# Performance work log

Measured on AMD Instinct MI355X. Metric: run time of the kernel, lower is better.

Reference implementation:

```python
import jax, jax.numpy as jnp
import numpy as np

B, N, L, H, K = 65536, 32, 8, 256, 8
RMIN, RMAX = -10.0, 10.0
MIN_BIN, MIN_SLOPE = 1e-4, 1e-4
P = 3 * K + 1  # params per feature per spline


def setup_inputs() -> dict:
    key = jax.random.key(0)
    ks = jax.random.split(key, 20)
    def rn(k, shape, s=0.05):
        return (jax.random.normal(k, shape, dtype=jnp.float32) * s)
    inp = {
        'x': jax.random.normal(ks[0], (B, N), dtype=jnp.float32),
        'sc_scale': 1.0 + rn(ks[1], (L, N)),
        'sc_shift': rn(ks[2], (L, N)),
        'W_in': rn(ks[3], (L, N, H)), 'b_in': rn(ks[4], (L, H)),
        'W1a': rn(ks[5], (L, H, H)), 'b1a': rn(ks[6], (L, H)),
        'W1b': rn(ks[7], (L, H, H)), 'b1b': rn(ks[8], (L, H)),
        'W2a': rn(ks[9], (L, H, H)), 'b2a': rn(ks[10], (L, H)),
        'W2b': rn(ks[11], (L, H, H)), 'b2b': rn(ks[12], (L, H)),
        'W_out': rn(ks[13], (L, H, N * P)), 'b_out': rn(ks[14], (L, N * P)),
        'perms': jnp.asarray(np.stack([np.random.RandomState(i).permutation(N) for i in range(L)]).astype(np.int32)),
    }
    return inp


def _conditioner(mx, Wi, bi, W1a, b1a, W1b, b1b, W2a, b2a, W2b, b2b, Wo, bo):
    # mx: [B, N] masked input -> [B, N, P] spline params
    h = mx @ Wi + bi
    r = jax.nn.relu(jax.nn.relu(h @ W1a + b1a) @ W1b + b1b)
    h = h + r
    r = jax.nn.relu(jax.nn.relu(h @ W2a + b2a) @ W2b + b2b)
    h = h + r
    h = jax.nn.relu(h)
    out = h @ Wo + bo
    return out.reshape(mx.shape[0], N, P)


def _rqs_forward(x, params):
    # x: [B, N]; params: [B, N, 3K+1]. distrax RationalQuadraticSpline forward.
    uw, uh, ud = params[..., :K], params[..., K:2 * K], params[..., 2 * K:]
    total = RMAX - RMIN
    w = jax.nn.softmax(uw, axis=-1) * (total - K * MIN_BIN) + MIN_BIN
    hgt = jax.nn.softmax(uh, axis=-1) * (total - K * MIN_BIN) + MIN_BIN
    zpad = jnp.zeros_like(w[..., :1])
    xp = RMIN + jnp.concatenate([zpad, jnp.cumsum(w, -1)], -1)   # [B,N,K+1]
    yp = RMIN + jnp.concatenate([zpad, jnp.cumsum(hgt, -1)], -1)
    offset = float(np.log(np.expm1(1.0 - MIN_SLOPE)))
    d = jax.nn.softplus(ud + offset) + MIN_SLOPE                  # [B,N,K+1]
    inside = (x > RMIN) & (x < RMAX)
    xc = jnp.clip(x, RMIN, RMAX)
    # per-element bin search (knot positions vary per element)
    idx = jnp.clip(jnp.sum((xc[..., None] >= xp).astype(jnp.int32), -1) - 1, 0, K - 1)
    g = lambda a, i: jnp.take_along_axis(a, i[..., None], -1)[..., 0]
    xk, xk1 = g(xp, idx), g(xp, idx + 1)
    yk, yk1 = g(yp, idx), g(yp, idx + 1)
    dk, dk1 = g(d, idx), g(d, idx + 1)
    bw = xk1 - xk
    bh = yk1 - yk
    s = bh / bw
    z = jnp.clip((xc - xk) / bw, 0.0, 1.0)
    zz = z * (1.0 - z)
    denom = s + (dk1 + dk - 2.0 * s) * zz
    y = yk + bh * (s * z * z + dk * zz) / denom
    ld = 2.0 * jnp.log(s) + jnp.log(dk1 * z * z + 2.0 * s * zz + dk * (1.0 - z) ** 2) - 2.0 * jnp.log(denom)
    return jnp.where(inside, y, x), jnp.where(inside, ld, 0.0)


def reference(x, sc_scale, sc_shift, W_in, b_in, W1a, b1a, W1b, b1b,
              W2a, b2a, W2b, b2b, W_out, b_out, perms):
    mask0 = (jnp.arange(N) % 2).astype(bool)  # True = identity (masked)
    logdet = jnp.zeros(x.shape[0], dtype=x.dtype)
    for i in range(L):
        # Permute
        x = x[:, perms[i]]
        # Scalar affine on all features (mask_all = all-False coupling)
        x = x * sc_scale[i] + sc_shift[i]
        logdet = logdet + jnp.sum(jnp.log(jnp.abs(sc_scale[i])))
        # RQ-spline masked coupling
        mask = mask0 if i % 2 == 0 else ~mask0
        mx = jnp.where(mask, x, 0.0)
        params = _conditioner(mx, W_in[i], b_in[i], W1a[i], b1a[i], W1b[i], b1b[i],
                              W2a[i], b2a[i], W2b[i], b2b[i], W_out[i], b_out[i])
        y, ld = _rqs_forward(x, params)
        x = jnp.where(mask, x, y)
        logdet = logdet + jnp.sum(jnp.where(mask, 0.0, ld), axis=-1)
    # standard-normal base log prob
    logp = -0.5 * jnp.sum(x * x, axis=-1) - 0.5 * N * float(np.log(2.0 * np.pi))
    return logp + logdet
```

## Files before the change

### kernel.cpp

```cpp
#include <hip/hip_runtime.h>
#include <hip/hip_bf16.h>

typedef __attribute__((ext_vector_type(8))) short bf16x8;
typedef __attribute__((ext_vector_type(16))) float f32x16;
typedef __attribute__((ext_vector_type(2))) float f32x2;

#define DEVFN __device__ __forceinline__

constexpr int NFEAT = 32, NLAYER = 8, HID = 256;
constexpr int HS  = 264;
constexpr int MXS = 40;
constexpr int XS  = 33;
constexpr int PS  = 132;
constexpr int WIN_E  = 2 * 256 * 16;
constexpr int WH_E   = 16 * 256 * 16;
constexpr int WOUT_E = 16 * 512 * 16;
constexpr int LAYER_E = WIN_E + 4 * WH_E + WOUT_E;
constexpr size_t WT_BYTES = (size_t)LAYER_E * NLAYER * 2;
constexpr size_t WS_NEEDED = WT_BYTES + NLAYER * 512 * 4 + 4;

constexpr float MIN_BIN = 1e-4f, MIN_SLOPE = 1e-4f;
constexpr float SOFTPLUS_OFF = 0.5411666f;
constexpr float WSCALE = 20.0f - 8.0f * MIN_BIN;

DEVFN unsigned short bf16r(float f) {
    unsigned u = __float_as_uint(f);
    u += 0x7fffu + ((u >> 16) & 1u);
    return (unsigned short)(u >> 16);
}
#if defined(__gfx950__) && __has_builtin(__builtin_amdgcn_cvt_pk_bf16_f32)
DEVFN unsigned pack2(float a, float b) {
    auto r = __builtin_amdgcn_cvt_pk_bf16_f32(a, b);
    return __builtin_bit_cast(unsigned, r);
}
#else
DEVFN unsigned pack2(float a, float b) {
    return (unsigned)bf16r(a) | ((unsigned)bf16r(b) << 16);
}
#endif
DEVFN float bflo(unsigned v) { return __uint_as_float(v << 16); }
DEVFN float bfhi(unsigned v) { return __uint_as_float(v & 0xffff0000u); }
DEVFN float frcp(float x) { return __builtin_amdgcn_rcpf(x); }
DEVFN f32x2 vmax0(f32x2 v) {
#if __has_builtin(__builtin_elementwise_max)
    return __builtin_elementwise_max(v, (f32x2){0.f, 0.f});
#else
    return (f32x2){fmaxf(v.x, 0.f), fmaxf(v.y, 0.f)};
#endif
}

__global__ __launch_bounds__(256) void prep_kernel(
    const float* __restrict__ Win, const float* __restrict__ W1a, const float* __restrict__ W1b,
    const float* __restrict__ W2a, const float* __restrict__ W2b, const float* __restrict__ Wout,
    const float* __restrict__ bout, const float* __restrict__ scS,
    short* __restrict__ wt, float* __restrict__ bo_t, float* __restrict__ sld)
{
    __shared__ float lb[16 * 800];
    const int b = blockIdx.x, t = threadIdx.x;
    if (b < 16) {
        int l = b >> 1, ks = b & 1;
        const float* src = Win + l * 32 * 256 + ks * 16 * 256;
#pragma unroll
        for (int i = 0; i < 16; i++) { int idx = t + i * 256; lb[idx] = src[idx]; }
        __syncthreads();
        short* dst = wt + (size_t)l * LAYER_E + ks * 4096;
#pragma unroll
        for (int i = 0; i < 16; i++) {
            int o = t + i * 256; int n = o >> 4, kk = o & 15;
            dst[o] = (short)bf16r(lb[kk * 256 + n]);
        }
    } else if (b < 528) {
        int id = b - 16; int l = id >> 6, mat = (id >> 4) & 3, ks = id & 15;
        const float* mats[4] = {W1a, W1b, W2a, W2b};
        const float* src = mats[mat] + l * 65536 + ks * 16 * 256;
#pragma unroll
        for (int i = 0; i < 16; i++) { int idx = t + i * 256; lb[idx] = src[idx]; }
        __syncthreads();
        short* dst = wt + (size_t)l * LAYER_E + WIN_E + mat * WH_E + ks * 4096;
#pragma unroll
        for (int i = 0; i < 16; i++) {
            int o = t + i * 256; int n = o >> 4, kk = o & 15;
            dst[o] = (short)bf16r(lb[kk * 256 + n]);
        }
    } else if (b < 656) {
        int id = b - 528; int l = id >> 4, ks = id & 15; int par = l & 1;
        const float* src = Wout + (size_t)l * 256 * 800 + ks * 16 * 800;
        for (int k = 0; k < 16; k++)
            for (int c = t; c < 800; c += 256) lb[k * 800 + c] = src[k * 800 + c];
        __syncthreads();
        short* dst = wt + (size_t)l * LAYER_E + WIN_E + 4 * WH_E + ks * 8192;
#pragma unroll
        for (int i = 0; i < 32; i++) {
            int o = t + i * 256; int c = o >> 4, kk = o & 15;
            int u = c >> 5, p = c & 31;
            float v = (p < 25) ? lb[kk * 800 + (2 * u + par) * 25 + p] : 0.0f;
            dst[o] = (short)bf16r(v);
        }
    } else {
#pragma unroll
        for (int i = 0; i < 16; i++) {
            int idx = t + i * 256;
            int l = idx >> 9, c = idx & 511, u = c >> 5, p = c & 31;
            bo_t[idx] = (p < 25) ? bout[l * 800 + (2 * u + (l & 1)) * 25 + p] : 0.0f;
        }
        lb[t] = logf(fabsf(scS[t]));
        __syncthreads();
        for (int s = 128; s > 0; s >>= 1) { if (t < s) lb[t] += lb[t + s]; __syncthreads(); }
        if (t == 0) *sld = lb[0];
    }
}

template<int KSTEPS, int NSUB>
DEVFN void gemm_flip(const short* __restrict__ wt, int ntot, int nbase,
                     const unsigned short* __restrict__ B, int bs,
                     f32x16 (&acc)[NSUB][2])
{
    constexpr int D = (KSTEPS < 4) ? KSTEPS : 4;
    const int lane = threadIdx.x & 63;
    const int l31 = lane & 31, l5 = lane >> 5;
    const bf16x8* __restrict__ w8 = (const bf16x8*)wt;
    const int wb = (nbase + l31) * 2 + l5;
    const int krow = ntot * 2;
    bf16x8 a[D][NSUB];
#pragma unroll
    for (int p = 0; p < D; p++)
#pragma unroll
        for (int s = 0; s < NSUB; s++) a[p][s] = w8[(size_t)p * krow + wb + s * 64];
    const unsigned short* bp = B + l31 * bs + l5 * 8;
#pragma unroll
    for (int k = 0; k < KSTEPS; k++) {
        bf16x8 b0 = *(const bf16x8*)(bp + k * 16);
        bf16x8 b1 = *(const bf16x8*)(bp + 32 * bs + k * 16);
#pragma unroll
        for (int s = 0; s < NSUB; s++) {
            acc[s][0] = __builtin_amdgcn_mfma_f32_32x32x16_bf16(a[k % D][s], b0, acc[s][0], 0, 0, 0);
            acc[s][1] = __builtin_amdgcn_mfma_f32_32x32x16_bf16(a[k % D][s], b1, acc[s][1], 0, 0, 0);
        }
        if (k + D < KSTEPS) {
#pragma unroll
            for (int s = 0; s < NSUB; s++) a[k % D][s] = w8[(size_t)(k + D) * krow + wb + s * 64];
        }
    }
}

DEVFN void binit(f32x16& a, const float* __restrict__ bias)
{
    const int q = (threadIdx.x >> 5) & 1;
    const float* bp = bias + 4 * q;
#pragma unroll
    for (int g = 0; g < 4; g++) {
        float4 b = *(const float4*)(bp + 8 * g);
        a[4*g+0] = b.x; a[4*g+1] = b.y; a[4*g+2] = b.z; a[4*g+3] = b.w;
    }
}

template<int MODE>
DEVFN void store_h(const f32x16& v, unsigned short* buf, int m0, int n0)
{
    const int lane = threadIdx.x & 63;
    const int m = m0 + (lane & 31);
    const int q = lane >> 5;
    unsigned short* rowp = buf + m * HS + n0 + 4 * q;
#pragma unroll
    for (int g = 0; g < 4; g++) {
        f32x2 r0 = {v[4*g+0], v[4*g+1]};
        f32x2 r1 = {v[4*g+2], v[4*g+3]};
        if (MODE >= 1) { r0 = vmax0(r0); r1 = vmax0(r1); }
        unsigned short* dst = rowp + 8 * g;
        if (MODE >= 2) {
            uint2 old = *(const uint2*)dst;
            r0 += (f32x2){bflo(old.x), bfhi(old.x)};
            r1 += (f32x2){bflo(old.y), bfhi(old.y)};
            if (MODE == 3) { r0 = vmax0(r0); r1 = vmax0(r1); }
        }
        uint2 pk;
        pk.x = pack2(r0.x, r0.y);
        pk.y = pack2(r1.x, r1.y);
        *(uint2*)dst = pk;
    }
}

DEVFN void store_p(const f32x16& v, float* pbuf, int m0, int c0)
{
    const int lane = threadIdx.x & 63;
    const int m = m0 + (lane & 31);
    const int q = lane >> 5;
    float* rowp = pbuf + m * PS + c0 + 4 * q;
#pragma unroll
    for (int g = 0; g < 4; g++)
        *(float4*)(rowp + 8 * g) = make_float4(v[4*g], v[4*g+1], v[4*g+2], v[4*g+3]);
}

__global__ __launch_bounds__(256, 2) void flow_kernel(
    const float* __restrict__ x_in, const float* __restrict__ scS, const float* __restrict__ scB,
    const float* __restrict__ bin, const float* __restrict__ b1a, const float* __restrict__ b1b,
    const float* __restrict__ b2a, const float* __restrict__ b2b,
    const int* __restrict__ perms,
    const short* __restrict__ wt, const float* __restrict__ bo_t, const float* __restrict__ sld,
    float* __restrict__ out)
{
    __shared__ __align__(16) unsigned short hS[64 * HS];
    __shared__ __align__(16) float uS[8448];
    __shared__ float xS[64 * XS];
    __shared__ float redS[256];

    const int tid = threadIdx.x;
    const int wave = tid >> 6;
    const size_t rowbase = (size_t)blockIdx.x * 64;
    unsigned short* tS  = (unsigned short*)uS;
    unsigned short* mxS = (unsigned short*)uS;
    float* pS = uS;

#pragma unroll
    for (int i = 0; i < 8; i++) {
        int g = tid + i * 256;
        xS[(g >> 5) * XS + (g & 31)] = x_in[rowbase * NFEAT + g];
    }
    float ld_acc = 0.0f;
    __syncthreads();

    const int nbase = wave * 64;

#pragma unroll 1
    for (int l = 0; l < NLAYER; l++) {
        const int par = l & 1;
        const short* wb = wt + (size_t)l * LAYER_E;

        {
            int j = tid & 31; int r0 = (tid >> 5) * 8;
            int pj = perms[l * 32 + j];
            float sc = scS[l * 32 + j], sh = scB[l * 32 + j];
            float vals[8];
#pragma unroll
            for (int r = 0; r < 8; r++) vals[r] = xS[(r0 + r) * XS + pj] * sc + sh;
            __syncthreads();
            int keep = ((j & 1) != par);
#pragma unroll
            for (int r = 0; r < 8; r++) {
                xS[(r0 + r) * XS + j] = vals[r];
                mxS[(r0 + r) * MXS + j] = keep ? bf16r(vals[r]) : (unsigned short)0;
            }
            __syncthreads();
        }
        {
            f32x16 acc[2][2];
            binit(acc[0][0], bin + l * 256 + nbase);      binit(acc[0][1], bin + l * 256 + nbase);
            binit(acc[1][0], bin + l * 256 + nbase + 32); binit(acc[1][1], bin + l * 256 + nbase + 32);
            gemm_flip<2, 2>(wb, 256, nbase, mxS, MXS, acc);
#pragma unroll
            for (int s = 0; s < 2; s++) {
                store_h<0>(acc[s][0], hS, 0,  nbase + s * 32);
                store_h<0>(acc[s][1], hS, 32, nbase + s * 32);
            }
            __syncthreads();
        }
        {
            f32x16 acc[2][2];
            binit(acc[0][0], b1a + l * 256 + nbase);      binit(acc[0][1], b1a + l * 256 + nbase);
            binit(acc[1][0], b1a + l * 256 + nbase + 32); binit(acc[1][1], b1a + l * 256 + nbase + 32);
            gemm_flip<16, 2>(wb + WIN_E, 256, nbase, hS, HS, acc);
#pragma unroll
            for (int s = 0; s < 2; s++) {
                store_h<1>(acc[s][0], tS, 0,  nbase + s * 32);
                store_h<1>(acc[s][1], tS, 32, nbase + s * 32);
            }
            __syncthreads();
        }
        {
            f32x16 acc[2][2];
            binit(acc[0][0], b1b + l * 256 + nbase);      binit(acc[0][1], b1b + l * 256 + nbase);
            binit(acc[1][0], b1b + l * 256 + nbase + 32); binit(acc[1][1], b1b + l * 256 + nbase + 32);
            gemm_flip<16, 2>(wb + WIN_E + WH_E, 256, nbase, tS, HS, acc);
#pragma unroll
            for (int s = 0; s < 2; s++) {
                store_h<2>(acc[s][0], hS, 0,  nbase + s * 32);
                store_h<2>(acc[s][1], hS, 32, nbase + s * 32);
            }
            __syncthreads();
        }
        {
            f32x16 acc[2][2];
            binit(acc[0][0], b2a + l * 256 + nbase);      binit(acc[0][1], b2a + l * 256 + nbase);
            binit(acc[1][0], b2a + l * 256 + nbase + 32); binit(acc[1][1], b2a + l * 256 + nbase + 32);
            gemm_flip<16, 2>(wb + WIN_E + 2 * WH_E, 256, nbase, hS, HS, acc);
#pragma unroll
            for (int s = 0; s < 2; s++) {
                store_h<1>(acc[s][0], tS, 0,  nbase + s * 32);
                store_h<1>(acc[s][1], tS, 32, nbase + s * 32);
            }
            __syncthreads();
        }
        {
            f32x16 acc[2][2];
            binit(acc[0][0], b2b + l * 256 + nbase);      binit(acc[0][1], b2b + l * 256 + nbase);
            binit(acc[1][0], b2b + l * 256 + nbase + 32); binit(acc[1][1], b2b + l * 256 + nbase + 32);
            gemm_flip<16, 2>(wb + WIN_E + 3 * WH_E, 256, nbase, tS, HS, acc);
#pragma unroll
            for (int s = 0; s < 2; s++) {
                store_h<3>(acc[s][0], hS, 0,  nbase + s * 32);
                store_h<3>(acc[s][1], hS, 32, nbase + s * 32);
            }
            __syncthreads();
        }
        const short* wo = wb + WIN_E + 4 * WH_E;
        for (int ch = 0; ch < 4; ch++) {
            {
                f32x16 acc[1][2];
                const float* bb = bo_t + l * 512 + ch * 128 + wave * 32;
                binit(acc[0][0], bb); binit(acc[0][1], bb);
                gemm_flip<16, 1>(wo, 512, ch * 128 + wave * 32, hS, HS, acc);
                store_p(acc[0][0], pS, 0,  wave * 32);
                store_p(acc[0][1], pS, 32, wave * 32);
            }
            __syncthreads();
            {
                int m = tid & 63, ul = tid >> 6;
                int n = 2 * (ch * 4 + ul) + par;
                float xv = xS[m * XS + n];
                const float* pp = pS + m * PS + ul * 32;
                float4 p0 = *(const float4*)(pp);
                float4 p1 = *(const float4*)(pp + 4);
                float4 p2 = *(const float4*)(pp + 8);
                float4 p3 = *(const float4*)(pp + 12);
                float4 p4 = *(const float4*)(pp + 16);
                float4 p5 = *(const float4*)(pp + 20);
                float p24 = pp[24];
                float uw[8] = {p0.x, p0.y, p0.z, p0.w, p1.x, p1.y, p1.z, p1.w};
                float uh[8] = {p2.x, p2.y, p2.z, p2.w, p3.x, p3.y, p3.z, p3.w};
                float ud[9] = {p4.x, p4.y, p4.z, p4.w, p5.x, p5.y, p5.z, p5.w, p24};

                float ew[8], eh[8], sw = 0.f, sh2 = 0.f;
#pragma unroll
                for (int i = 0; i < 8; i++) { ew[i] = __expf(uw[i]); sw += ew[i]; }
#pragma unroll
                for (int i = 0; i < 8; i++) { eh[i] = __expf(uh[i]); sh2 += eh[i]; }
                float fw = WSCALE * frcp(sw), fh = WSCALE * frcp(sh2);
                float w[8], hh[8];
#pragma unroll
                for (int i = 0; i < 8; i++) { w[i] = fmaf(ew[i], fw, MIN_BIN); hh[i] = fmaf(eh[i], fh, MIN_BIN); }

                bool inside = (xv > -10.0f) && (xv < 10.0f);
                float xc = fminf(fmaxf(xv, -10.0f), 10.0f);
                float cx = -10.0f + w[0], cy = -10.0f + hh[0];
                float xk = -10.0f, yk = -10.0f, bw = w[0], bh = hh[0];
                float udk = ud[0], udk1 = ud[1];
#pragma unroll
                for (int i = 1; i < 8; i++) {
                    bool take = (xc >= cx);
                    if (take) { xk = cx; yk = cy; bw = w[i]; bh = hh[i]; udk = ud[i]; udk1 = ud[i + 1]; }
                    cx += w[i]; cy += hh[i];
                }
                float dk  = __logf(1.f + __expf(udk  + SOFTPLUS_OFF)) + MIN_SLOPE;
                float dk1 = __logf(1.f + __expf(udk1 + SOFTPLUS_OFF)) + MIN_SLOPE;
                float ibw = frcp(bw);
                float s = bh * ibw;
                float z = fminf(fmaxf((xc - xk) * ibw, 0.0f), 1.0f);
                float omz = 1.0f - z;
                float zz = z * omz;
                float denom = fmaf(dk1 + dk - 2.0f * s, zz, s);
                float idenom = frcp(denom);
                float y = fmaf(bh * fmaf(s * z, z, dk * zz), idenom, yk);
                float num = fmaf(dk1 * z, z, fmaf(2.0f * s, zz, dk * omz * omz));
                float ldv = 2.0f * __logf(s * idenom) + __logf(num);
                xS[m * XS + n] = inside ? y : xv;
                ld_acc += inside ? ldv : 0.0f;
            }
            __syncthreads();
        }
    }
    {
        int m = tid & 63, jg = tid >> 6;
        float s2 = 0.f;
#pragma unroll
        for (int j = 0; j < 8; j++) { float v = xS[m * XS + jg * 8 + j]; s2 += v * v; }
        redS[tid] = ld_acc - 0.5f * s2;
        __syncthreads();
        if (tid < 64) {
            float tot = redS[tid] + redS[tid + 64] + redS[tid + 128] + redS[tid + 192]
                      + *sld - 29.406033062549525f;
            out[rowbase + tid] = tot;
        }
    }
}

extern "C" void kernel_launch(void* const* d_in, const int* in_sizes, int n_in,
                              void* d_out, int out_size, void* d_ws, size_t ws_size,
                              hipStream_t stream) {
    if (ws_size < WS_NEEDED) return;
    const float* x    = (const float*)d_in[0];
    const float* scS  = (const float*)d_in[1];
    const float* scB  = (const float*)d_in[2];
    const float* Win  = (const float*)d_in[3];
    const float* bin  = (const float*)d_in[4];
    const float* W1a  = (const float*)d_in[5];
    const float* b1a  = (const float*)d_in[6];
    const float* W1b  = (const float*)d_in[7];
    const float* b1b  = (const float*)d_in[8];
    const float* W2a  = (const float*)d_in[9];
    const float* b2a  = (const float*)d_in[10];
    const float* W2b  = (const float*)d_in[11];
    const float* b2b  = (const float*)d_in[12];
    const float* Wout = (const float*)d_in[13];
    const float* bout = (const float*)d_in[14];
    const int* perms  = (const int*)d_in[15];

    short* wt   = (short*)d_ws;
    float* bo_t = (float*)((char*)d_ws + WT_BYTES);
    float* sld  = bo_t + NLAYER * 512;

    prep_kernel<<<657, 256, 0, stream>>>(Win, W1a, W1b, W2a, W2b, Wout, bout, scS, wt, bo_t, sld);
    flow_kernel<<<65536 / 64, 256, 0, stream>>>(x, scS, scB, bin, b1a, b1b, b2a, b2b,
                                                perms, wt, bo_t, sld, (float*)d_out);
}
```

Before: 598.7 us.

## Fuse output GEMM with spline evaluation in registers via lane shuffles

```diff
diff --git a/kernel.cpp b/kernel.cpp
--- a/kernel.cpp
+++ b/kernel.cpp
@@ -11,7 +11,6 @@
 constexpr int HS  = 264;
 constexpr int MXS = 40;
 constexpr int XS  = 33;
-constexpr int PS  = 132;
 constexpr int WIN_E  = 2 * 256 * 16;
 constexpr int WH_E   = 16 * 256 * 16;
 constexpr int WOUT_E = 16 * 512 * 16;
@@ -110,12 +109,12 @@
     }
 }
 
-template<int KSTEPS, int NSUB>
+template<int KSTEPS, int NSUB, int DEPTH>
 DEVFN void gemm_flip(const short* __restrict__ wt, int ntot, int nbase,
                      const unsigned short* __restrict__ B, int bs,
                      f32x16 (&acc)[NSUB][2])
 {
-    constexpr int D = (KSTEPS < 4) ? KSTEPS : 4;
+    constexpr int D = (KSTEPS < DEPTH) ? KSTEPS : DEPTH;
     const int lane = threadIdx.x & 63;
     const int l31 = lane & 31, l5 = lane >> 5;
     const bf16x8* __restrict__ w8 = (const bf16x8*)wt;
@@ -180,17 +179,6 @@
     }
 }
 
-DEVFN void store_p(const f32x16& v, float* pbuf, int m0, int c0)
-{
-    const int lane = threadIdx.x & 63;
-    const int m = m0 + (lane & 31);
-    const int q = lane >> 5;
-    float* rowp = pbuf + m * PS + c0 + 4 * q;
-#pragma unroll
-    for (int g = 0; g < 4; g++)
-        *(float4*)(rowp + 8 * g) = make_float4(v[4*g], v[4*g+1], v[4*g+2], v[4*g+3]);
-}
-
 __global__ __launch_bounds__(256, 2) void flow_kernel(
     const float* __restrict__ x_in, const float* __restrict__ scS, const float* __restrict__ scB,
     const float* __restrict__ bin, const float* __restrict__ b1a, const float* __restrict__ b1b,
@@ -200,16 +188,17 @@
     float* __restrict__ out)
 {
     __shared__ __align__(16) unsigned short hS[64 * HS];
-    __shared__ __align__(16) float uS[8448];
+    __shared__ __align__(16) unsigned short uS[64 * HS];
     __shared__ float xS[64 * XS];
     __shared__ float redS[256];
 
     const int tid = threadIdx.x;
     const int wave = tid >> 6;
+    const int lane = tid & 63;
+    const int q = lane >> 5;
     const size_t rowbase = (size_t)blockIdx.x * 64;
-    unsigned short* tS  = (unsigned short*)uS;
-    unsigned short* mxS = (unsigned short*)uS;
-    float* pS = uS;
+    unsigned short* tS  = uS;
+    unsigned short* mxS = uS;
 
 #pragma unroll
     for (int i = 0; i < 8; i++) {
@@ -246,7 +235,7 @@
             f32x16 acc[2][2];
             binit(acc[0][0], bin + l * 256 + nbase);      binit(acc[0][1], bin + l * 256 + nbase);
             binit(acc[1][0], bin + l * 256 + nbase + 32); binit(acc[1][1], bin + l * 256 + nbase + 32);
-            gemm_flip<2, 2>(wb, 256, nbase, mxS, MXS, acc);
+            gemm_flip<2, 2, 2>(wb, 256, nbase, mxS, MXS, acc);
 #pragma unroll
             for (int s = 0; s < 2; s++) {
                 store_h<0>(acc[s][0], hS, 0,  nbase + s * 32);
@@ -258,7 +247,7 @@
             f32x16 acc[2][2];
             binit(acc[0][0], b1a + l * 256 + nbase);      binit(acc[0][1], b1a + l * 256 + nbase);
             binit(acc[1][0], b1a + l * 256 + nbase + 32); binit(acc[1][1], b1a + l * 256 + nbase + 32);
-            gemm_flip<16, 2>(wb + WIN_E, 256, nbase, hS, HS, acc);
+            gemm_flip<16, 2, 4>(wb + WIN_E, 256, nbase, hS, HS, acc);
 #pragma unroll
             for (int s = 0; s < 2; s++) {
                 store_h<1>(acc[s][0], tS, 0,  nbase + s * 32);
@@ -270,7 +259,7 @@
             f32x16 acc[2][2];
             binit(acc[0][0], b1b + l * 256 + nbase);      binit(acc[0][1], b1b + l * 256 + nbase);
             binit(acc[1][0], b1b + l * 256 + nbase + 32); binit(acc[1][1], b1b + l * 256 + nbase + 32);
-            gemm_flip<16, 2>(wb + WIN_E + WH_E, 256, nbase, tS, HS, acc);
+            gemm_flip<16, 2, 4>(wb + WIN_E + WH_E, 256, nbase, tS, HS, acc);
 #pragma unroll
             for (int s = 0; s < 2; s++) {
                 store_h<2>(acc[s][0], hS, 0,  nbase + s * 32);
@@ -282,7 +271,7 @@
             f32x16 acc[2][2];
             binit(acc[0][0], b2a + l * 256 + nbase);      binit(acc[0][1], b2a + l * 256 + nbase);
             binit(acc[1][0], b2a + l * 256 + nbase + 32); binit(acc[1][1], b2a + l * 256 + nbase + 32);
-            gemm_flip<16, 2>(wb + WIN_E + 2 * WH_E, 256, nbase, hS, HS, acc);
+            gemm_flip<16, 2, 4>(wb + WIN_E + 2 * WH_E, 256, nbase, hS, HS, acc);
 #pragma unroll
             for (int s = 0; s < 2; s++) {
                 store_h<1>(acc[s][0], tS, 0,  nbase + s * 32);
@@ -294,7 +283,7 @@
             f32x16 acc[2][2];
             binit(acc[0][0], b2b + l * 256 + nbase);      binit(acc[0][1], b2b + l * 256 + nbase);
             binit(acc[1][0], b2b + l * 256 + nbase + 32); binit(acc[1][1], b2b + l * 256 + nbase + 32);
-            gemm_flip<16, 2>(wb + WIN_E + 3 * WH_E, 256, nbase, tS, HS, acc);
+            gemm_flip<16, 2, 4>(wb + WIN_E + 3 * WH_E, 256, nbase, tS, HS, acc);
 #pragma unroll
             for (int s = 0; s < 2; s++) {
                 store_h<3>(acc[s][0], hS, 0,  nbase + s * 32);
@@ -302,38 +291,42 @@
             }
             __syncthreads();
         }
-        const short* wo = wb + WIN_E + 4 * WH_E;
-        for (int ch = 0; ch < 4; ch++) {
-            {
-                f32x16 acc[1][2];
-                const float* bb = bo_t + l * 512 + ch * 128 + wave * 32;
-                binit(acc[0][0], bb); binit(acc[0][1], bb);
-                gemm_flip<16, 1>(wo, 512, ch * 128 + wave * 32, hS, HS, acc);
-                store_p(acc[0][0], pS, 0,  wave * 32);
-                store_p(acc[0][1], pS, 32, wave * 32);
-            }
-            __syncthreads();
-            {
-                int m = tid & 63, ul = tid >> 6;
-                int n = 2 * (ch * 4 + ul) + par;
-                float xv = xS[m * XS + n];
-                const float* pp = pS + m * PS + ul * 32;
-                float4 p0 = *(const float4*)(pp);
-                float4 p1 = *(const float4*)(pp + 4);
-                float4 p2 = *(const float4*)(pp + 8);
-                float4 p3 = *(const float4*)(pp + 12);
-                float4 p4 = *(const float4*)(pp + 16);
-                float4 p5 = *(const float4*)(pp + 20);
-                float p24 = pp[24];
-                float uw[8] = {p0.x, p0.y, p0.z, p0.w, p1.x, p1.y, p1.z, p1.w};
-                float uh[8] = {p2.x, p2.y, p2.z, p2.w, p3.x, p3.y, p3.z, p3.w};
-                float ud[9] = {p4.x, p4.y, p4.z, p4.w, p5.x, p5.y, p5.z, p5.w, p24};
-
+        {
+            const short* wo = wb + WIN_E + 4 * WH_E;
+            f32x16 acc[4][2];
+            const float* bb = bo_t + l * 512 + wave * 128;
+#pragma unroll
+            for (int s = 0; s < 4; s++) { binit(acc[s][0], bb + s * 32); binit(acc[s][1], bb + s * 32); }
+            gemm_flip<16, 4, 2>(wo, 512, wave * 128, hS, HS, acc);
+
+#pragma unroll
+            for (int s = 0; s < 4; s++) {
+                float exch[16];
+#pragma unroll
+                for (int i = 0; i < 16; i++) {
+                    float snd = q ? acc[s][0][i] : acc[s][1][i];
+                    exch[i] = __shfl_xor(snd, 32, 64);
+                }
+                float A0[16], A1[16];
+#pragma unroll
+                for (int i = 0; i < 16; i++) {
+                    float kept = q ? acc[s][1][i] : acc[s][0][i];
+                    A0[i] = q ? exch[i] : kept;
+                    A1[i] = q ? kept : exch[i];
+                }
+                float P[25];
+#pragma unroll
+                for (int p = 0; p < 25; p++) {
+                    int rg = (p & 3) + 4 * (p >> 3);
+                    P[p] = ((p >> 2) & 1) ? A1[rg] : A0[rg];
+                }
+                int n = 2 * (4 * wave + s) + par;
+                float xv = xS[lane * XS + n];
                 float ew[8], eh[8], sw = 0.f, sh2 = 0.f;
 #pragma unroll
-                for (int i = 0; i < 8; i++) { ew[i] = __expf(uw[i]); sw += ew[i]; }
-#pragma unroll
-                for (int i = 0; i < 8; i++) { eh[i] = __expf(uh[i]); sh2 += eh[i]; }
+                for (int i = 0; i < 8; i++) { ew[i] = __expf(P[i]); sw += ew[i]; }
+#pragma unroll
+                for (int i = 0; i < 8; i++) { eh[i] = __expf(P[8 + i]); sh2 += eh[i]; }
                 float fw = WSCALE * frcp(sw), fh = WSCALE * frcp(sh2);
                 float w[8], hh[8];
 #pragma unroll
@@ -343,26 +336,26 @@
                 float xc = fminf(fmaxf(xv, -10.0f), 10.0f);
                 float cx = -10.0f + w[0], cy = -10.0f + hh[0];
                 float xk = -10.0f, yk = -10.0f, bw = w[0], bh = hh[0];
-                float udk = ud[0], udk1 = ud[1];
+                float udk = P[16], udk1 = P[17];
 #pragma unroll
                 for (int i = 1; i < 8; i++) {
                     bool take = (xc >= cx);
-                    if (take) { xk = cx; yk = cy; bw = w[i]; bh = hh[i]; udk = ud[i]; udk1 = ud[i + 1]; }
+                    if (take) { xk = cx; yk = cy; bw = w[i]; bh = hh[i]; udk = P[16 + i]; udk1 = P[17 + i]; }
                     cx += w[i]; cy += hh[i];
                 }
                 float dk  = __logf(1.f + __expf(udk  + SOFTPLUS_OFF)) + MIN_SLOPE;
                 float dk1 = __logf(1.f + __expf(udk1 + SOFTPLUS_OFF)) + MIN_SLOPE;
                 float ibw = frcp(bw);
-                float s = bh * ibw;
+                float s_ = bh * ibw;
                 float z = fminf(fmaxf((xc - xk) * ibw, 0.0f), 1.0f);
                 float omz = 1.0f - z;
                 float zz = z * omz;
-                float denom = fmaf(dk1 + dk - 2.0f * s, zz, s);
+                float denom = fmaf(dk1 + dk - 2.0f * s_, zz, s_);
                 float idenom = frcp(denom);
-                float y = fmaf(bh * fmaf(s * z, z, dk * zz), idenom, yk);
-                float num = fmaf(dk1 * z, z, fmaf(2.0f * s, zz, dk * omz * omz));
-                float ldv = 2.0f * __logf(s * idenom) + __logf(num);
-                xS[m * XS + n] = inside ? y : xv;
+                float y = fmaf(bh * fmaf(s_ * z, z, dk * zz), idenom, yk);
+                float num = fmaf(dk1 * z, z, fmaf(2.0f * s_, zz, dk * omz * omz));
+                float ldv = 2.0f * __logf(s_ * idenom) + __logf(num);
+                xS[lane * XS + n] = inside ? y : xv;
                 ld_acc += inside ? ldv : 0.0f;
             }
             __syncthreads();
```

Result: faster. 573.9 us (-4.1%).
